# Optimization experiments

Hardware: AMD Instinct MI355X
Metric: run time of the kernel (lower is better)

Reference implementation:

```python
import jax, jax.numpy as jnp
import numpy as np
from functools import partial

NP = 1024      # particles
T = 128        # timesteps
CUR_MIN, CUR_MAX = -2.0, 4.0
E_CRIT = 29000.0
F_STD = 0.005
G_STD = 0.01
NU = 1.0 / (G_STD * np.sqrt(2.0 * np.pi))

# VoC battery open-circuit-voltage curve constants
V_L, V_0 = -1.59614486, 4.13646328
GAMMA, ALPHA, BETA = 0.63726463, 1.40174122, 2.54478965


def voc(soc):
    return (V_L + (V_0 - V_L) * jnp.exp(GAMMA * (soc - 1.0))
            + ALPHA * V_L * (soc - 1.0)
            + (1.0 - ALPHA) * V_L * (jnp.exp(-BETA) - jnp.exp(-BETA * jnp.sqrt(soc))))


def setup_inputs() -> dict:
    key = jax.random.key(0)
    ks = jax.random.split(key, 11)
    soc_init = jax.random.uniform(ks[0], (NP, 1), jnp.float32, 0.3, 1.0)
    current = jax.random.normal(ks[1], (1, T), jnp.float32) * 0.5 + 1.0
    voltage_measured = 3.7 + 0.1 * jax.random.normal(ks[2], (1, T), jnp.float32)
    W1 = jax.random.normal(ks[3], (2, 1024), jnp.float32) / np.sqrt(2.0)
    b1 = jnp.zeros((1024,), jnp.float32)
    W2 = jax.random.normal(ks[4], (1024, 512), jnp.float32) / np.sqrt(1024.0)
    b2 = jnp.zeros((512,), jnp.float32)
    W3 = jax.random.normal(ks[5], (512, 1), jnp.float32) / np.sqrt(512.0)
    b3 = jnp.zeros((1,), jnp.float32)
    noise = jax.random.normal(ks[6], (T, NP, 1), jnp.float32)  # unit-std process noise
    u = jax.random.uniform(ks[7], (T,), jnp.float32)           # systematic-resampling offsets
    return {"soc_init": soc_init, "current": current, "voltage_measured": voltage_measured,
            "W1": W1, "b1": b1, "W2": W2, "b2": b2, "W3": W3, "b3": b3,
            "noise": noise, "u": u}


def _forward(soc_init, current, voltage_measured, W1, b1, W2, b2, W3, b3, noise, u):
    n = soc_init.shape[0]

    def mlp(x):  # [n,2] -> [n,1]
        z = jax.nn.sigmoid(x @ W1 + b1)
        z = jax.nn.sigmoid(z @ W2 + b2)
        return z @ W3 + b3

    def scale_I(I):
        return (I - CUR_MIN) / (CUR_MAX - CUR_MIN)

    cur = current[0]                       # [T]
    vmeas = voltage_measured[0]            # [T]
    cur_prev = jnp.concatenate([cur[:1], cur[:-1]])  # first step reuses current[0,0]

    def step(soc, xs):
        c_prev, c_t, vm, eps, ut = xs
        # --- prediction with previous current ---
        I = jnp.broadcast_to(c_prev, soc.shape)
        Z = mlp(jnp.concatenate([soc, scale_I(I)], axis=1))
        V = voc(soc) - I * Z
        soc = soc - I * V / E_CRIT + eps * F_STD
        soc = jnp.clip(soc, 1e-10, 1.0)
        # --- measurement update with current at t ---
        I = jnp.broadcast_to(c_t, soc.shape)
        sI = scale_I(I)
        Z = mlp(jnp.concatenate([soc, sI], axis=1))
        V = voc(soc) - I * Z
        logW = np.log(NU) - 0.5 * ((V - vm) / G_STD) ** 2  # [n,1]
        w = jnp.exp(logW - jnp.max(logW))[:, 0]
        wn = w / jnp.sum(w)
        # systematic resampling (deterministic given offset ut)
        cdf = jnp.cumsum(wn)
        pos = (ut + jnp.arange(n, dtype=jnp.float32)) / n
        idx = jnp.clip(jnp.searchsorted(cdf, pos), 0, n - 1)
        soc = soc[idx]
        # --- post-resample evaluation ---
        Z = mlp(jnp.concatenate([soc, sI], axis=1))
        V = voc(soc) - I * Z
        mse = jnp.mean((V - vm) ** 2)
        return soc, (mse, V[:, 0], soc[:, 0])

    soc0 = soc_init.astype(jnp.float32)
    _, (mses, Vs, socs) = jax.lax.scan(step, soc0, (cur_prev, cur, vmeas, noise, u))
    loss = jnp.mean(mses)        # == sum_t mse_t / T
    voltage = Vs.T               # [n, T]
    soc_hist = socs.T            # [n, T]
    return loss, voltage, soc_hist


def reference(soc_init, current, voltage_measured, W1, b1, W2, b2, W3, b3, noise, u):
    return _forward(soc_init, current, voltage_measured, W1, b1, W2, b2, W3, b3, noise, u)
```

## Files before the change

### kernel.cpp

```cpp
#include <hip/hip_runtime.h>
#include <stdint.h>

typedef __attribute__((ext_vector_type(8))) short short8;
typedef __attribute__((ext_vector_type(4))) float floatx4;

#define DONE_MAGIC 0x600DF00Du


__device__ __forceinline__ float sigm(float x) { return 1.0f / (1.0f + expf(-x)); }

__device__ __forceinline__ float vocf(float s) {
  const float V_L = -1.59614486f, V_0 = 4.13646328f;
  const float GAM = 0.63726463f, ALP = 1.40174122f, BET = 2.54478965f;
  return V_L + (V_0 - V_L) * expf(GAM * (s - 1.0f)) + ALP * V_L * (s - 1.0f)
       + (1.0f - ALP) * V_L * (expf(-BET) - expf(-BET * sqrtf(s)));
}

__device__ __forceinline__ unsigned short f2bf(float f) {
  unsigned u = __float_as_uint(f);
  u += 0x7FFFu + ((u >> 16) & 1u);
  return (unsigned short)(u >> 16);
}
__device__ __forceinline__ float bf2f(unsigned short b) {
  return __uint_as_float(((unsigned)b) << 16);
}

__device__ __forceinline__ float interp_c(const float* ctab, float s) {
  float f = s * 31.0f;
  float jf = fminf(floorf(f), 30.0f);
  int j = (int)jf;
  float u = f - jf;
  const float4 c = *(const float4*)&ctab[j * 4];
  return fmaf(fmaf(fmaf(c.w, u, c.z), u, c.y), u, c.x);
}

__device__ __forceinline__ int send_bl(float c, float u) {
  float C = c * 1024.0f;
  float sf = floorf(C - u);
  sf += (u + (sf + 1.0f) <= C) ? 1.0f : 0.0f;
  sf -= (u + sf > C) ? 1.0f : 0.0f;
  return (int)sf;
}

__device__ __forceinline__ float fast_exp2(float x) {
  float r;
  asm("v_exp_f32 %0, %1" : "=v"(r) : "v"(x));
  return r;
}


template<int C, int RM>
__device__ __forceinline__ float dpp_add_f(float x) {
  return __int_as_float(__builtin_amdgcn_update_dpp(0, __float_as_int(x), C, RM, 0xF, false));
}
template<int C, int RM>
__device__ __forceinline__ float dpp_old_f(float x) {
  return __int_as_float(__builtin_amdgcn_update_dpp(__float_as_int(x), __float_as_int(x), C, RM, 0xF, false));
}
template<int C, int RM>
__device__ __forceinline__ int dpp_old_i(int x) {
  return __builtin_amdgcn_update_dpp(x, x, C, RM, 0xF, false);
}
__device__ __forceinline__ float dpp_wshr1_f0(float x) {
  return __int_as_float(__builtin_amdgcn_update_dpp(0, __float_as_int(x), 0x138, 0xF, 0xF, true));
}
__device__ __forceinline__ int dpp_wshr1_i(int x, int old) {
  return __builtin_amdgcn_update_dpp(old, x, 0x138, 0xF, 0xF, false);
}
__device__ __forceinline__ int dpp_wshl1_i(int x, int old) {
  return __builtin_amdgcn_update_dpp(old, x, 0x130, 0xF, 0xF, false);
}

__device__ __forceinline__ float wave_iscan_add(float x) {
  x += dpp_add_f<0x111, 0xF>(x);
  x += dpp_add_f<0x112, 0xF>(x);
  x += dpp_add_f<0x114, 0xF>(x);
  x += dpp_add_f<0x118, 0xF>(x);
  x += dpp_add_f<0x142, 0xA>(x);
  x += dpp_add_f<0x143, 0xC>(x);
  return x;
}
__device__ __forceinline__ float wave_max_bcast(float x) {
  x = fmaxf(x, dpp_old_f<0xB1,  0xF>(x));
  x = fmaxf(x, dpp_old_f<0x4E,  0xF>(x));
  x = fmaxf(x, dpp_old_f<0x141, 0xF>(x));
  x = fmaxf(x, dpp_old_f<0x140, 0xF>(x));
  x = fmaxf(x, dpp_old_f<0x142, 0xA>(x));
  x = fmaxf(x, dpp_old_f<0x143, 0xC>(x));
  return __int_as_float(__builtin_amdgcn_readlane(__float_as_int(x), 63));
}
__device__ __forceinline__ int wave_iscan_max(int x) {
  x = max(x, dpp_old_i<0x111, 0xF>(x));
  x = max(x, dpp_old_i<0x112, 0xF>(x));
  x = max(x, dpp_old_i<0x114, 0xF>(x));
  x = max(x, dpp_old_i<0x118, 0xF>(x));
  x = max(x, dpp_old_i<0x142, 0xA>(x));
  x = max(x, dpp_old_i<0x143, 0xC>(x));
  return x;
}

__device__ __forceinline__ float rdlane_f(float x, int lane) {
  return __int_as_float(__builtin_amdgcn_readlane(__float_as_int(x), lane));
}

__device__ __forceinline__ void bar_lds() {
  asm volatile("s_waitcnt lgkmcnt(0)" ::: "memory");
  __builtin_amdgcn_s_barrier();
  asm volatile("" ::: "memory");
}


__global__ void __launch_bounds__(256)
k1_swizzle(const float* __restrict__ W2g, short* __restrict__ w2hiG, short* __restrict__ w2loG)
{
  int bid = blockIdx.x, tid = threadIdx.x;
  int pg = bid & 15, ng = bid >> 4;
  int u = pg * 256 + tid;
  int kb = u >> 7, l = u & 63, nt = (u >> 6) & 1, kq = l >> 4;
  int col = ng * 32 + nt * 16 + (l & 15);
  short8 hi8, lo8;
  #pragma unroll
  for (int j = 0; j < 8; j++) {
    int k = kb * 32 + kq * 8 + j;
    float w = W2g[k * 512 + col];
    unsigned short h = f2bf(w);
    hi8[j] = (short)h;
    lo8[j] = (short)f2bf(w - bf2f(h));
  }
  size_t off = ((size_t)ng * 4096 + u) * 8;
  *(short8*)(w2hiG + off) = hi8;
  *(short8*)(w2loG + off) = lo8;
}


__global__ void __launch_bounds__(256)
k2_gemm(const float* __restrict__ curg, const float* __restrict__ W1g,
        const float* __restrict__ b1g, const float* __restrict__ b2g,
        const float* __restrict__ W3g, const short* __restrict__ w2hiG,
        const short* __restrict__ w2loG, float* __restrict__ part)
{
  __shared__ short w2S[32768];
  __shared__ float b2S[32], w3S[32];

  const int tid = threadIdx.x, bid = blockIdx.x;
  const int ng = bid & 15, rtg = bid >> 4;
  const int wv = tid >> 6, ln = tid & 63;
  const int kq = ln >> 4;

  {
    const short* srcH = w2hiG + (size_t)ng * 32768;
    for (int i = tid; i < 4096; i += 256)
      *(short8*)(w2S + i * 8) = *(const short8*)(srcH + i * 8);
    if (tid < 32) { b2S[tid] = b2g[ng * 32 + tid]; w3S[tid] = W3g[ng * 32 + tid]; }
  }
  __syncthreads();

  const short* loG = w2loG + (size_t)ng * 32768;
  const int c = ln & 15, q = ln >> 4;
  const float b20 = b2S[c], b21 = b2S[16 + c];
  const float w30 = w3S[c], w31 = w3S[16 + c];

  for (int jj = 0; jj < 3; jj++) {
    int rt = rtg + 32 * jj;
    if (rt >= 72) break;
    int pt = rt * 4 + wv;
    unsigned r = pt * 16 + (ln & 15);
    unsigned t = r / 36u;
    int i = (int)(r - t * 36u);
    float soc = (float)(i - 1) * (1.0f / 31.0f);
    float sI = (curg[t] + 2.0f) / 6.0f;

    floatx4 acc0 = {0.f, 0.f, 0.f, 0.f};
    floatx4 acc1 = {0.f, 0.f, 0.f, 0.f};

    for (int kb = 0; kb < 32; kb++) {
      int k0 = kb * 32 + kq * 8;
      floatx4 wa0 = *(const floatx4*)(W1g + k0);
      floatx4 wa1 = *(const floatx4*)(W1g + k0 + 4);
      floatx4 wb0 = *(const floatx4*)(W1g + 1024 + k0);
      floatx4 wb1 = *(const floatx4*)(W1g + 1024 + k0 + 4);
      floatx4 bb0 = *(const floatx4*)(b1g + k0);
      floatx4 bb1 = *(const floatx4*)(b1g + k0 + 4);
      short8 ah, al;
      #pragma unroll
      for (int j = 0; j < 4; j++) {
        float x = soc * wa0[j] + sI * wb0[j] + bb0[j];
        float z = __builtin_amdgcn_rcpf(1.0f + __expf(-x));
        unsigned short h = f2bf(z);
        ah[j] = (short)h;
        al[j] = (short)f2bf(z - bf2f(h));
      }
      #pragma unroll
      for (int j = 0; j < 4; j++) {
        float x = soc * wa1[j] + sI * wb1[j] + bb1[j];
        float z = __builtin_amdgcn_rcpf(1.0f + __expf(-x));
        unsigned short h = f2bf(z);
        ah[4 + j] = (short)h;
        al[4 + j] = (short)f2bf(z - bf2f(h));
      }
      short8 bh0 = *(const short8*)(w2S + (kb * 2 + 0) * 512 + ln * 8);
      short8 bh1 = *(const short8*)(w2S + (kb * 2 + 1) * 512 + ln * 8);
      short8 bl0 = *(const short8*)(loG + (kb * 2 + 0) * 512 + ln * 8);
      short8 bl1 = *(const short8*)(loG + (kb * 2 + 1) * 512 + ln * 8);
      acc0 = __builtin_amdgcn_mfma_f32_16x16x32_bf16(ah, bh0, acc0, 0, 0, 0);
      acc1 = __builtin_amdgcn_mfma_f32_16x16x32_bf16(ah, bh1, acc1, 0, 0, 0);
      acc0 = __builtin_amdgcn_mfma_f32_16x16x32_bf16(ah, bl0, acc0, 0, 0, 0);
      acc1 = __builtin_amdgcn_mfma_f32_16x16x32_bf16(ah, bl1, acc1, 0, 0, 0);
      acc0 = __builtin_amdgcn_mfma_f32_16x16x32_bf16(al, bh0, acc0, 0, 0, 0);
      acc1 = __builtin_amdgcn_mfma_f32_16x16x32_bf16(al, bh1, acc1, 0, 0, 0);
    }

    #pragma unroll
    for (int r2 = 0; r2 < 4; r2++) {
      float v = w30 * sigm(acc0[r2] + b20) + w31 * sigm(acc1[r2] + b21);
      v += __shfl_xor(v, 1);
      v += __shfl_xor(v, 2);
      v += __shfl_xor(v, 4);
      v += __shfl_xor(v, 8);
      if (c == 0) part[(size_t)(pt * 16 + q * 4 + r2) * 16 + ng] = v;
    }
  }
}


__device__ __forceinline__ int swzi(int j) { return ((j & 3) << 8) | (j >> 2); }

__global__ void __launch_bounds__(256)
pf_seq(const float* __restrict__ soc_init, const float* __restrict__ curg,
       const float* __restrict__ vmeasg, const float* __restrict__ noise_g,
       const float* __restrict__ u_g, const float* __restrict__ part,
       const float* __restrict__ b3g, float* __restrict__ ctabG,
       unsigned* __restrict__ doneG, float* __restrict__ outp,
       unsigned* __restrict__ flag)
{
  __shared__ float ctabS[15872];
  __shared__ float2 pvS[2][1024];
  __shared__ int   markS[1024] __attribute__((aligned(16)));
  __shared__ int   chunkS[4] __attribute__((aligned(16)));
  __shared__ float2 msS[4] __attribute__((aligned(16)));
  __shared__ float lossS[4];
  __shared__ float Vrow[36];

  const int bid = blockIdx.x;
  const int tid = threadIdx.x;

  {
    if (tid < 36) {
      const float* p = part + (size_t)(bid * 36 + tid) * 16;
      float s = 0.f;
      #pragma unroll
      for (int i = 0; i < 16; i++) s += p[i];
      float Z = s + b3g[0];
      float node = (float)(tid - 1) * (1.0f / 31.0f);
      float nodc = fmaxf(node, 1e-10f);
      Vrow[tid] = vocf(nodc) - curg[bid] * Z;
    }
    __syncthreads();
    if (tid < 31) {
      float n0 = Vrow[tid], n1 = Vrow[tid + 1], n2 = Vrow[tid + 2], n3 = Vrow[tid + 3];
      float c0 = n1;
      float c1 = (-2.0f * n0 - 3.0f * n1 + 6.0f * n2 - n3) * (1.0f / 6.0f);
      float c2 = (n0 - 2.0f * n1 + n2) * 0.5f;
      float c3 = (-n0 + 3.0f * (n1 - n2) + n3) * (1.0f / 6.0f);
      *(float4*)&ctabG[(bid * 31 + tid) * 4] = make_float4(c0, c1, c2, c3);
    }
    __threadfence();
    __syncthreads();
    if (tid == 0)
      __hip_atomic_store(&doneG[bid], DONE_MAGIC, __ATOMIC_RELEASE, __HIP_MEMORY_SCOPE_AGENT);
  }

  if (bid != 0) {
    while (__hip_atomic_load(flag, __ATOMIC_RELAXED, __HIP_MEMORY_SCOPE_AGENT) != DONE_MAGIC) {
      __builtin_amdgcn_s_sleep(64);
    }
    return;
  }

  if (tid < 128) {
    while (__hip_atomic_load(&doneG[tid], __ATOMIC_ACQUIRE, __HIP_MEMORY_SCOPE_AGENT) != DONE_MAGIC)
      __builtin_amdgcn_s_sleep(1);
  }
  __syncthreads();

  const int w = tid >> 6, l = tid & 63;
  const int p0 = tid * 4;

  #pragma unroll
  for (int k = 0; k < 16; k++) {
    int i = tid + 256 * k;
    if (i < 3968) *(float4*)&ctabS[i * 4] = *(const float4*)&ctabG[i * 4];
  }
  float curA = curg[l],   curB = curg[64 + l];
  float vmA  = vmeasg[l], vmB  = vmeasg[64 + l];
  float uA   = u_g[l],    uB   = u_g[64 + l];
  *(int4*)&markS[p0] = make_int4(-1, -1, -1, -1);
  if (tid < 4) chunkS[tid] = -1;

  float sp0, sp1, sp2, sp3;
  {
    float4 s4 = *(const float4*)(soc_init + p0);
    float4 n4 = *(const float4*)(noise_g + p0);
    bar_lds();
    float c0 = rdlane_f(curA, 0);
    float c02 = c0 * (1.0f / 29000.0f);
    float spv[4];
    #pragma unroll
    for (int r = 0; r < 4; r++) {
      float si = ((const float*)&s4)[r];
      float V0 = interp_c(ctabS, si);
      float spn = fmaf(((const float*)&n4)[r], 0.005f, fmaf(-c02, V0, si));
      spv[r] = __builtin_amdgcn_fmed3f(spn, 1e-10f, 1.0f);
    }
    sp0 = spv[0]; sp1 = spv[1]; sp2 = spv[2]; sp3 = spv[3];
  }

  float lossAcc = 0.0f;
  float* vbase = outp + 1 + p0 * 128;
  float* sbase = vbase + 131072;

  for (int t = 0; t < 128; t++) {
    const float* ctab = ctabS + t * 124;
    const int cb = t & 1;
    float cI, vm, ut;
    if (t < 64) { cI = rdlane_f(curA, t); vm = rdlane_f(vmA, t); ut = rdlane_f(uA, t); }
    else        { cI = rdlane_f(curB, t - 64); vm = rdlane_f(vmB, t - 64); ut = rdlane_f(uB, t - 64); }
    float cI2 = cI * (1.0f / 29000.0f);

    int tn = (t < 127) ? t + 1 : 127;
    float4 noi4 = *(const float4*)(noise_g + tn * 1024 + p0);

    float V10 = interp_c(ctab, sp0);
    float V11 = interp_c(ctab, sp1);
    float V12 = interp_c(ctab, sp2);
    float V13 = interp_c(ctab, sp3);
    pvS[cb][tid]       = make_float2(sp0, V10);
    pvS[cb][256 + tid] = make_float2(sp1, V11);
    pvS[cb][512 + tid] = make_float2(sp2, V12);
    pvS[cb][768 + tid] = make_float2(sp3, V13);
    float d0 = V10 - vm, d1 = V11 - vm, d2 = V12 - vm, d3 = V13 - vm;
    float lw0 = d0 * d0 * -7213.4755594f;
    float lw1 = d1 * d1 * -7213.4755594f;
    float lw2 = d2 * d2 * -7213.4755594f;
    float lw3 = d3 * d3 * -7213.4755594f;

    float lmax = fmaxf(fmaxf(lw0, lw1), fmaxf(lw2, lw3));
    float mw = wave_max_bcast(lmax);
    float pr0, pr1, pr2, pr3, acc;
    {
      float w0 = fast_exp2(lw0 - mw); acc = w0;    pr0 = acc;
      float w1 = fast_exp2(lw1 - mw); acc += w1;   pr1 = acc;
      float w2 = fast_exp2(lw2 - mw); acc += w2;   pr2 = acc;
      float w3 = fast_exp2(lw3 - mw); acc += w3;   pr3 = acc;
    }
    float isc = wave_iscan_add(acc);
    if (l == 63) msS[w] = make_float2(mw, isc);
    bar_lds();

    float4 ms01 = *(const float4*)&msS[0];
    float4 ms23 = *(const float4*)&msS[2];
    float m = fmaxf(fmaxf(ms01.x, ms01.z), fmaxf(ms23.x, ms23.z));
    float f0 = fast_exp2(ms01.x - m), f1 = fast_exp2(ms01.z - m);
    float f2 = fast_exp2(ms23.x - m), f3 = fast_exp2(ms23.z - m);
    float t0 = ms01.y * f0, t1 = ms01.w * f1, t2 = ms23.y * f2, t3 = ms23.w * f3;
    float total = (t0 + t1) + (t2 + t3);
    float woff = (w > 0 ? t0 : 0.0f) + (w > 1 ? t1 : 0.0f) + (w > 2 ? t2 : 0.0f);
    float fw = (w == 0) ? f0 : ((w == 1) ? f1 : ((w == 2) ? f2 : f3));
    float exclw = dpp_wshr1_f0(isc);
    float rS = 1.0f / total;

    int se0 = send_bl(fmaf(exclw + pr0, fw, woff) * rS, ut);
    int se1 = send_bl(fmaf(exclw + pr1, fw, woff) * rS, ut);
    int se2 = send_bl(fmaf(exclw + pr2, fw, woff) * rS, ut);
    int se3 = send_bl(fmaf(exclw + pr3, fw, woff) * rS, ut);

    int nxt = dpp_wshl1_i(se0, se3);
    int tbase = t << 10;
    if (tid == 0 && se0 >= 0) { markS[0] = tbase; atomicMax(&chunkS[0], tbase); }
    if (se1 > se0 && se0 < 1023) {
      int s = se0 + 1, tg = tbase | (p0 + 1);
      markS[swzi(s)] = tg; atomicMax(&chunkS[s >> 8], tg);
    }
    if (se2 > se1 && se1 < 1023) {
      int s = se1 + 1, tg = tbase | (p0 + 2);
      markS[swzi(s)] = tg; atomicMax(&chunkS[s >> 8], tg);
    }
    if (se3 > se2 && se2 < 1023) {
      int s = se2 + 1, tg = tbase | (p0 + 3);
      markS[swzi(s)] = tg; atomicMax(&chunkS[s >> 8], tg);
    }
    if (l != 63) {
      if (nxt > se3 && se3 < 1023) {
        int s = se3 + 1, tg = tbase | (p0 + 4);
        markS[swzi(s)] = tg; atomicMax(&chunkS[s >> 8], tg);
      }
    } else {
      if (se3 < 1023) {
        int s = se3 + 1;
        int tg = (tid == 255) ? (tbase | 1023) : (tbase | (p0 + 4));
        atomicMax(&markS[swzi(s)], tg); atomicMax(&chunkS[s >> 8], tg);
      }
    }
    bar_lds();

    int mk0 = markS[tid],       mk1 = markS[256 + tid];
    int mk2 = markS[512 + tid], mk3 = markS[768 + tid];
    int4 ch4 = *(const int4*)chunkS;
    int q0 = mk0;
    int q1 = max(q0, mk1);
    int q2 = max(q1, mk2);
    int q3 = max(q2, mk3);
    int iscI = wave_iscan_max(q3);
    int ex = dpp_wshr1_i(iscI, -1);
    if (w > 0) ex = max(ex, ch4.x);
    if (w > 1) ex = max(ex, ch4.y);
    if (w > 2) ex = max(ex, ch4.z);

    int o0 = max(ex, q0) & 1023, o1 = max(ex, q1) & 1023;
    int o2 = max(ex, q2) & 1023, o3 = max(ex, q3) & 1023;
    float2 g0 = pvS[cb][swzi(o0)];
    float2 g1 = pvS[cb][swzi(o1)];
    float2 g2 = pvS[cb][swzi(o2)];
    float2 g3 = pvS[cb][swzi(o3)];

    vbase[t]       = g0.y;  sbase[t]       = g0.x;
    vbase[128 + t] = g1.y;  sbase[128 + t] = g1.x;
    vbase[256 + t] = g2.y;  sbase[256 + t] = g2.x;
    vbase[384 + t] = g3.y;  sbase[384 + t] = g3.x;

    float e0 = g0.y - vm, e1 = g1.y - vm, e2 = g2.y - vm, e3 = g3.y - vm;
    lossAcc = fmaf(e0, e0, lossAcc);
    lossAcc = fmaf(e1, e1, lossAcc);
    lossAcc = fmaf(e2, e2, lossAcc);
    lossAcc = fmaf(e3, e3, lossAcc);
    const float* nz = (const float*)&noi4;
    sp0 = __builtin_amdgcn_fmed3f(fmaf(nz[0], 0.005f, fmaf(-cI2, g0.y, g0.x)), 1e-10f, 1.0f);
    sp1 = __builtin_amdgcn_fmed3f(fmaf(nz[1], 0.005f, fmaf(-cI2, g1.y, g1.x)), 1e-10f, 1.0f);
    sp2 = __builtin_amdgcn_fmed3f(fmaf(nz[2], 0.005f, fmaf(-cI2, g2.y, g2.x)), 1e-10f, 1.0f);
    sp3 = __builtin_amdgcn_fmed3f(fmaf(nz[3], 0.005f, fmaf(-cI2, g3.y, g3.x)), 1e-10f, 1.0f);
  }

  float ls = wave_iscan_add(lossAcc);
  if (l == 63) lossS[w] = ls;
  bar_lds();
  if (tid == 0) {
    outp[0] = (lossS[0] + lossS[1] + lossS[2] + lossS[3]) * (1.0f / 131072.0f);
    __hip_atomic_store(flag, DONE_MAGIC, __ATOMIC_RELEASE, __HIP_MEMORY_SCOPE_AGENT);
  }
}


extern "C" void kernel_launch(void* const* d_in, const int* in_sizes, int n_in,
                              void* d_out, int out_size, void* d_ws, size_t ws_size,
                              hipStream_t stream) {
  const float* soc_init = (const float*)d_in[0];
  const float* cur      = (const float*)d_in[1];
  const float* vmeas    = (const float*)d_in[2];
  const float* W1       = (const float*)d_in[3];
  const float* b1       = (const float*)d_in[4];
  const float* W2       = (const float*)d_in[5];
  const float* b2       = (const float*)d_in[6];
  const float* W3       = (const float*)d_in[7];
  const float* b3       = (const float*)d_in[8];
  const float* noise    = (const float*)d_in[9];
  const float* u        = (const float*)d_in[10];
  float* out = (float*)d_out;
  char* ws = (char*)d_ws;

  short* w2hi    = (short*)ws;
  short* w2lo    = (short*)(ws + (1 << 20));
  float* part    = (float*)(ws + (2 << 20));
  char*  p3      = ws + (2 << 20) + 4608 * 16 * 4;
  float* ctabG   = (float*)p3;
  unsigned* doneG = (unsigned*)(p3 + 3968 * 16);
  unsigned* flag  = (unsigned*)(p3 + 3968 * 16 + 512);

  k1_swizzle<<<256, 256, 0, stream>>>(W2, w2hi, w2lo);
  k2_gemm<<<512, 256, 0, stream>>>(cur, W1, b1, b2, W3, w2hi, w2lo, part);
  pf_seq<<<128, 256, 0, stream>>>(soc_init, cur, vmeas, noise, u, part, b3,
                                  ctabG, doneG, out, flag);
}
```

Measured before the change: 383.4 us.

## Restructure GEMM tiling and coalesce output writes via staging plus parallel transpose

The GEMM kernel now launches one block per row tile and per group of four column groups, reusing the computed layer-1 activations across four N-groups. It reads W2 hi/lo straight from global memory instead of staging a slice in LDS. The sequential particle-filter block now writes voltage and SOC history as coalesced float4 rows into a [T,NP] workspace. Idle blocks, after the completion flag is set, transpose that workspace into the [NP,T] output through LDS tiles. This removes strided scalar stores from the serial critical path, at the cost of an extra transpose pass and more global traffic for W2 in the GEMM.

```diff
diff --git a/kernel.cpp b/kernel.cpp
--- a/kernel.cpp
+++ b/kernel.cpp
@@ -139,80 +139,82 @@
         const float* __restrict__ W3g, const short* __restrict__ w2hiG,
         const short* __restrict__ w2loG, float* __restrict__ part)
 {
-  __shared__ short w2S[32768];
-  __shared__ float b2S[32], w3S[32];
-
   const int tid = threadIdx.x, bid = blockIdx.x;
-  const int ng = bid & 15, rtg = bid >> 4;
+  const int nh = bid / 72;
+  const int rt = bid - nh * 72;
   const int wv = tid >> 6, ln = tid & 63;
   const int kq = ln >> 4;
-
-  {
-    const short* srcH = w2hiG + (size_t)ng * 32768;
-    for (int i = tid; i < 4096; i += 256)
-      *(short8*)(w2S + i * 8) = *(const short8*)(srcH + i * 8);
-    if (tid < 32) { b2S[tid] = b2g[ng * 32 + tid]; w3S[tid] = W3g[ng * 32 + tid]; }
-  }
-  __syncthreads();
-
-  const short* loG = w2loG + (size_t)ng * 32768;
   const int c = ln & 15, q = ln >> 4;
-  const float b20 = b2S[c], b21 = b2S[16 + c];
-  const float w30 = w3S[c], w31 = w3S[16 + c];
-
-  for (int jj = 0; jj < 3; jj++) {
-    int rt = rtg + 32 * jj;
-    if (rt >= 72) break;
-    int pt = rt * 4 + wv;
-    unsigned r = pt * 16 + (ln & 15);
-    unsigned t = r / 36u;
-    int i = (int)(r - t * 36u);
-    float soc = (float)(i - 1) * (1.0f / 31.0f);
-    float sI = (curg[t] + 2.0f) / 6.0f;
-
-    floatx4 acc0 = {0.f, 0.f, 0.f, 0.f};
-    floatx4 acc1 = {0.f, 0.f, 0.f, 0.f};
-
-    for (int kb = 0; kb < 32; kb++) {
-      int k0 = kb * 32 + kq * 8;
-      floatx4 wa0 = *(const floatx4*)(W1g + k0);
-      floatx4 wa1 = *(const floatx4*)(W1g + k0 + 4);
-      floatx4 wb0 = *(const floatx4*)(W1g + 1024 + k0);
-      floatx4 wb1 = *(const floatx4*)(W1g + 1024 + k0 + 4);
-      floatx4 bb0 = *(const floatx4*)(b1g + k0);
-      floatx4 bb1 = *(const floatx4*)(b1g + k0 + 4);
-      short8 ah, al;
-      #pragma unroll
-      for (int j = 0; j < 4; j++) {
-        float x = soc * wa0[j] + sI * wb0[j] + bb0[j];
-        float z = __builtin_amdgcn_rcpf(1.0f + __expf(-x));
-        unsigned short h = f2bf(z);
-        ah[j] = (short)h;
-        al[j] = (short)f2bf(z - bf2f(h));
-      }
-      #pragma unroll
-      for (int j = 0; j < 4; j++) {
-        float x = soc * wa1[j] + sI * wb1[j] + bb1[j];
-        float z = __builtin_amdgcn_rcpf(1.0f + __expf(-x));
-        unsigned short h = f2bf(z);
-        ah[4 + j] = (short)h;
-        al[4 + j] = (short)f2bf(z - bf2f(h));
-      }
-      short8 bh0 = *(const short8*)(w2S + (kb * 2 + 0) * 512 + ln * 8);
-      short8 bh1 = *(const short8*)(w2S + (kb * 2 + 1) * 512 + ln * 8);
-      short8 bl0 = *(const short8*)(loG + (kb * 2 + 0) * 512 + ln * 8);
-      short8 bl1 = *(const short8*)(loG + (kb * 2 + 1) * 512 + ln * 8);
-      acc0 = __builtin_amdgcn_mfma_f32_16x16x32_bf16(ah, bh0, acc0, 0, 0, 0);
-      acc1 = __builtin_amdgcn_mfma_f32_16x16x32_bf16(ah, bh1, acc1, 0, 0, 0);
-      acc0 = __builtin_amdgcn_mfma_f32_16x16x32_bf16(ah, bl0, acc0, 0, 0, 0);
-      acc1 = __builtin_amdgcn_mfma_f32_16x16x32_bf16(ah, bl1, acc1, 0, 0, 0);
-      acc0 = __builtin_amdgcn_mfma_f32_16x16x32_bf16(al, bh0, acc0, 0, 0, 0);
-      acc1 = __builtin_amdgcn_mfma_f32_16x16x32_bf16(al, bh1, acc1, 0, 0, 0);
-    }
-
+
+  const int pt = rt * 4 + wv;
+  unsigned r = pt * 16 + c;
+  unsigned t = r / 36u;
+  int i = (int)(r - t * 36u);
+  float soc = (float)(i - 1) * (1.0f / 31.0f);
+  float sI = (curg[t] + 2.0f) / 6.0f;
+
+  floatx4 acc[4][2];
+  #pragma unroll
+  for (int g = 0; g < 4; g++) {
+    acc[g][0] = (floatx4){0.f, 0.f, 0.f, 0.f};
+    acc[g][1] = (floatx4){0.f, 0.f, 0.f, 0.f};
+  }
+
+  const size_t ngBase = (size_t)(nh * 4) * 32768;
+
+  for (int kb = 0; kb < 32; kb++) {
+    int k0 = kb * 32 + kq * 8;
+    floatx4 wa0 = *(const floatx4*)(W1g + k0);
+    floatx4 wa1 = *(const floatx4*)(W1g + k0 + 4);
+    floatx4 wb0 = *(const floatx4*)(W1g + 1024 + k0);
+    floatx4 wb1 = *(const floatx4*)(W1g + 1024 + k0 + 4);
+    floatx4 bb0 = *(const floatx4*)(b1g + k0);
+    floatx4 bb1 = *(const floatx4*)(b1g + k0 + 4);
+    short8 ah, al;
+    #pragma unroll
+    for (int j = 0; j < 4; j++) {
+      float x = soc * wa0[j] + sI * wb0[j] + bb0[j];
+      float z = __builtin_amdgcn_rcpf(1.0f + __expf(-x));
+      unsigned short h = f2bf(z);
+      ah[j] = (short)h;
+      al[j] = (short)f2bf(z - bf2f(h));
+    }
+    #pragma unroll
+    for (int j = 0; j < 4; j++) {
+      float x = soc * wa1[j] + sI * wb1[j] + bb1[j];
+      float z = __builtin_amdgcn_rcpf(1.0f + __expf(-x));
+      unsigned short h = f2bf(z);
+      ah[4 + j] = (short)h;
+      al[4 + j] = (short)f2bf(z - bf2f(h));
+    }
+
+    const short* hi = w2hiG + ngBase + (size_t)(kb * 2) * 512 + ln * 8;
+    const short* lo = w2loG + ngBase + (size_t)(kb * 2) * 512 + ln * 8;
+    #pragma unroll
+    for (int g = 0; g < 4; g++) {
+      const short* hg = hi + (size_t)g * 32768;
+      const short* lg = lo + (size_t)g * 32768;
+      short8 bh0 = *(const short8*)(hg);
+      short8 bh1 = *(const short8*)(hg + 512);
+      short8 bl0 = *(const short8*)(lg);
+      short8 bl1 = *(const short8*)(lg + 512);
+      acc[g][0] = __builtin_amdgcn_mfma_f32_16x16x32_bf16(ah, bh0, acc[g][0], 0, 0, 0);
+      acc[g][1] = __builtin_amdgcn_mfma_f32_16x16x32_bf16(ah, bh1, acc[g][1], 0, 0, 0);
+      acc[g][0] = __builtin_amdgcn_mfma_f32_16x16x32_bf16(ah, bl0, acc[g][0], 0, 0, 0);
+      acc[g][1] = __builtin_amdgcn_mfma_f32_16x16x32_bf16(ah, bl1, acc[g][1], 0, 0, 0);
+      acc[g][0] = __builtin_amdgcn_mfma_f32_16x16x32_bf16(al, bh0, acc[g][0], 0, 0, 0);
+      acc[g][1] = __builtin_amdgcn_mfma_f32_16x16x32_bf16(al, bh1, acc[g][1], 0, 0, 0);
+    }
+  }
+
+  #pragma unroll
+  for (int g = 0; g < 4; g++) {
+    int ng = nh * 4 + g;
+    float b20 = b2g[ng * 32 + c],      b21 = b2g[ng * 32 + 16 + c];
+    float w30 = W3g[ng * 32 + c],      w31 = W3g[ng * 32 + 16 + c];
     #pragma unroll
     for (int r2 = 0; r2 < 4; r2++) {
-      float v = w30 * sigm(acc0[r2] + b20) + w31 * sigm(acc1[r2] + b21);
+      float v = w30 * sigm(acc[g][0][r2] + b20) + w31 * sigm(acc[g][1][r2] + b21);
       v += __shfl_xor(v, 1);
       v += __shfl_xor(v, 2);
       v += __shfl_xor(v, 4);
@@ -230,7 +232,8 @@
        const float* __restrict__ vmeasg, const float* __restrict__ noise_g,
        const float* __restrict__ u_g, const float* __restrict__ part,
        const float* __restrict__ b3g, float* __restrict__ ctabG,
-       unsigned* __restrict__ doneG, float* __restrict__ outp,
+       unsigned* __restrict__ doneG, float* __restrict__ vout,
+       float* __restrict__ sout, float* __restrict__ outp,
        unsigned* __restrict__ flag)
 {
   __shared__ float ctabS[15872];
@@ -271,8 +274,29 @@
   }
 
   if (bid != 0) {
-    while (__hip_atomic_load(flag, __ATOMIC_RELAXED, __HIP_MEMORY_SCOPE_AGENT) != DONE_MAGIC) {
-      __builtin_amdgcn_s_sleep(64);
+    while (__hip_atomic_load(flag, __ATOMIC_ACQUIRE, __HIP_MEMORY_SCOPE_AGENT) != DONE_MAGIC) {
+      __builtin_amdgcn_s_sleep(32);
+    }
+    if (bid <= 32) {
+      int sl = bid - 1;
+      int arr = sl & 1, pg = sl >> 1;
+      const float* src = arr ? sout : vout;
+      float* dst = outp + 1 + arr * 131072;
+      float* tile = ctabS;
+      int p0g = pg * 64;
+      #pragma unroll 4
+      for (int s = 0; s < 32; s++) {
+        int tt = s * 4 + (tid >> 6);
+        int p = tid & 63;
+        tile[tt * 65 + p] = src[tt * 1024 + p0g + p];
+      }
+      __syncthreads();
+      #pragma unroll 4
+      for (int s = 0; s < 32; s++) {
+        int pl = s * 2 + (tid >> 7);
+        int tt = tid & 127;
+        dst[(p0g + pl) * 128 + tt] = tile[tt * 65 + pl];
+      }
     }
     return;
   }
@@ -316,8 +340,6 @@
   }
 
   float lossAcc = 0.0f;
-  float* vbase = outp + 1 + p0 * 128;
-  float* sbase = vbase + 131072;
 
   for (int t = 0; t < 128; t++) {
     const float* ctab = ctabS + t * 124;
@@ -423,10 +445,8 @@
     float2 g2 = pvS[cb][swzi(o2)];
     float2 g3 = pvS[cb][swzi(o3)];
 
-    vbase[t]       = g0.y;  sbase[t]       = g0.x;
-    vbase[128 + t] = g1.y;  sbase[128 + t] = g1.x;
-    vbase[256 + t] = g2.y;  sbase[256 + t] = g2.x;
-    vbase[384 + t] = g3.y;  sbase[384 + t] = g3.x;
+    *(float4*)(vout + t * 1024 + p0) = make_float4(g0.y, g1.y, g2.y, g3.y);
+    *(float4*)(sout + t * 1024 + p0) = make_float4(g0.x, g1.x, g2.x, g3.x);
 
     float e0 = g0.y - vm, e1 = g1.y - vm, e2 = g2.y - vm, e3 = g3.y - vm;
     lossAcc = fmaf(e0, e0, lossAcc);
@@ -467,16 +487,18 @@
   float* out = (float*)d_out;
   char* ws = (char*)d_ws;
 
-  short* w2hi    = (short*)ws;
-  short* w2lo    = (short*)(ws + (1 << 20));
-  float* part    = (float*)(ws + (2 << 20));
-  char*  p3      = ws + (2 << 20) + 4608 * 16 * 4;
-  float* ctabG   = (float*)p3;
+  short* w2hi     = (short*)ws;
+  short* w2lo     = (short*)(ws + (1 << 20));
+  float* part     = (float*)(ws + (2 << 20));
+  char*  p3       = ws + (2 << 20) + 4608 * 16 * 4;
+  float* ctabG    = (float*)p3;
   unsigned* doneG = (unsigned*)(p3 + 3968 * 16);
   unsigned* flag  = (unsigned*)(p3 + 3968 * 16 + 512);
+  float* vout     = (float*)(p3 + 3968 * 16 + 1024);
+  float* sout     = (float*)(p3 + 3968 * 16 + 1024 + (512 << 10));
 
   k1_swizzle<<<256, 256, 0, stream>>>(W2, w2hi, w2lo);
-  k2_gemm<<<512, 256, 0, stream>>>(cur, W1, b1, b2, W3, w2hi, w2lo, part);
+  k2_gemm<<<288, 256, 0, stream>>>(cur, W1, b1, b2, W3, w2hi, w2lo, part);
   pf_seq<<<128, 256, 0, stream>>>(soc_init, cur, vmeas, noise, u, part, b3,
-                                  ctabG, doneG, out, flag);
-}
+                                  ctabG, doneG, vout, sout, out, flag);
+}
```

After: 341.7 us. 1.12x faster.
